# Optimization experiments

Measured on AMD Instinct MI355X. Metric: run time of the kernel, lower is better.

Reference implementation:

```python
import jax, jax.numpy as jnp
import numpy as np

SHRINK_THRES = 0.0025
EPS_SHRINK = 1e-12
EPS_NORM = 1e-12


def setup_inputs() -> dict:
    key = jax.random.key(0)
    k1, k2 = jax.random.split(key)
    B, C, H, W = 32, 256, 32, 32
    mem_dim, fea_dim = 2000, 256
    x = jax.random.normal(k1, (B, C, H, W), dtype=jnp.float32)
    stdv = 1.0 / np.sqrt(fea_dim)
    memMatrix = jax.random.uniform(k2, (mem_dim, fea_dim), dtype=jnp.float32,
                                   minval=-stdv, maxval=stdv)
    return {"x": x, "memMatrix": memMatrix}


def _hard_shrink_relu(a, lambd, eps=EPS_SHRINK):
    # relu(a - lambd) * a / (|a - lambd| + eps)
    return jax.nn.relu(a - lambd) * a / (jnp.abs(a - lambd) + eps)


def reference(x, memMatrix):
    B, C, H, W = x.shape
    mem_dim = memMatrix.shape[0]
    # [B,C,H,W] -> [B,H,W,C] -> [N,C]
    q = jnp.transpose(x, (0, 2, 3, 1)).reshape(-1, C)
    # attention addressing: [N, mem_dim]
    att = q @ memMatrix.T
    att = jax.nn.softmax(att, axis=1)
    # hard shrinkage + L1 renormalize
    att = _hard_shrink_relu(att, SHRINK_THRES)
    denom = jnp.maximum(jnp.sum(jnp.abs(att), axis=1, keepdims=True), EPS_NORM)
    att = att / denom
    # memory read: [N, C]
    out = att @ memMatrix
    # reshape back: y [B,C,H,W], att [B,mem_dim,H,W]
    y = jnp.transpose(out.reshape(B, H, W, C), (0, 3, 1, 2))
    att_map = jnp.transpose(att.reshape(B, H, W, mem_dim), (0, 3, 1, 2))
    return y, att_map
```

## Files before the change

kernel.cpp:

```cpp
#include <hip/hip_runtime.h>

#define B_   32
#define C_   256
#define HW_  1024
#define N_   32768
#define M_   2000
#define MP_  2048
#define K_   256

typedef __attribute__((ext_vector_type(8))) _Float16 f16x8;
typedef __attribute__((ext_vector_type(4))) float f32x4;

#define KCAP 32
#define AP   264

#define MFMA16(a, b, c) __builtin_amdgcn_mfma_f32_16x16x32_f16(a, b, c, 0, 0, 0)

__global__ void prep_memS_kernel(const float* __restrict__ mem,
                                 _Float16* __restrict__ mhs) {
  int m = blockIdx.x;
  int p = threadIdx.x;
  int c = ((p & 15) << 4) | (p >> 4);
  float v = (m < M_) ? mem[m * K_ + c] * 64.0f : 0.0f;
  _Float16 h = (_Float16)v;
  _Float16 l = (_Float16)(v - (float)h);
  int ks = p >> 5, kk = p & 31;
  int sh = (kk >> 3) ^ (m & 7);
  int sl = ((kk >> 3) + 4) ^ (m & 7);
  size_t base = ((size_t)ks * MP_ + m) * 64;
  mhs[base + sh * 8 + (kk & 7)] = h;
  mhs[base + sl * 8 + (kk & 7)] = l;
}

__global__ __launch_bounds__(512, 1) void fused_kernel(
    const float* __restrict__ x, const _Float16* __restrict__ mhs,
    const float* __restrict__ mem,
    float* __restrict__ y, float* __restrict__ att) {
  __shared__ _Float16 Bs[2][256 * 64];
  __shared__ _Float16 Ahs[32][AP];
  __shared__ _Float16 Als[32][AP];
  __shared__ float S_part[8][32];
  __shared__ float Sthr[32];
  __shared__ float inv_s[32];
  __shared__ unsigned int kcnt[32];
  __shared__ unsigned int km[32][KCAP];
  __shared__ float kp[32][KCAP];

  const int tid   = threadIdx.x;
  const int lane  = tid & 63;
  const int wave  = tid >> 6;
  const int row16 = lane & 15;
  const int quad  = lane >> 4;
  const int r7    = row16 & 7;
  const int n0  = blockIdx.x * 32;
  const int b   = n0 >> 10;
  const int hw0 = n0 & 1023;

  float (*xs)[33] = (float (*)[33])&Bs[0][0];

  {
    const int c = tid >> 1;
    const int h16 = (tid & 1) * 16;
    const float* src = x + ((size_t)b * C_ + c) * HW_ + hw0 + h16;
#pragma unroll
    for (int i = 0; i < 4; ++i)
      *(f32x4*)(&xs[c][h16 + i * 4]) = *(const f32x4*)(src + i * 4);
  }
  if (tid < 32) kcnt[tid] = 0;
  __syncthreads();

  {
    const int nl = tid >> 4;
    const int g  = tid & 15;
    f16x8 hi0, hi1, lo0, lo1;
#pragma unroll
    for (int u = 0; u < 8; ++u) {
      float v = xs[u * 16 + g][nl];
      _Float16 h = (_Float16)v;
      hi0[u] = h; lo0[u] = (_Float16)(v - (float)h);
    }
#pragma unroll
    for (int u = 0; u < 8; ++u) {
      float v = xs[(u + 8) * 16 + g][nl];
      _Float16 h = (_Float16)v;
      hi1[u] = h; lo1[u] = (_Float16)(v - (float)h);
    }
    *(f16x8*)(&Ahs[nl][g * 16])     = hi0;
    *(f16x8*)(&Ahs[nl][g * 16 + 8]) = hi1;
    *(f16x8*)(&Als[nl][g * 16])     = lo0;
    *(f16x8*)(&Als[nl][g * 16 + 8]) = lo1;
  }
  __syncthreads();

#define STAGE(bufidx, unit) do {                                              \
    const _Float16* gs_ = mhs + (size_t)(unit) * 16384;                       \
    _Float16* ld_ = &Bs[bufidx][0];                                           \
    _Pragma("unroll")                                                         \
    for (int i_ = 0; i_ < 4; ++i_) {                                          \
      __builtin_amdgcn_global_load_lds(                                       \
        (const __attribute__((address_space(1))) unsigned int*)(gs_ + (i_ * 512 + tid) * 8), \
        (__attribute__((address_space(3))) unsigned int*)(ld_ + (i_ * 512 + tid) * 8),       \
        16, 0, 0);                                                            \
    }                                                                         \
  } while (0)

  STAGE(0, 0);
  __syncthreads();

  f32x4 acc[8][2][2];
#pragma unroll
  for (int ch = 0; ch < 8; ++ch)
#pragma unroll
    for (int nf = 0; nf < 2; ++nf)
#pragma unroll
      for (int mf = 0; mf < 2; ++mf) acc[ch][nf][mf] = (f32x4){0.f, 0.f, 0.f, 0.f};

  const int mA = wave * 32;
  const int sH = (quad ^ r7) * 8;
  const int sL = ((4 | quad) ^ r7) * 8;

#pragma unroll 1
  for (int ks = 0; ks < 8; ++ks) {
    f16x8 ah[2], al[2];
#pragma unroll
    for (int nf = 0; nf < 2; ++nf) {
      ah[nf] = *(const f16x8*)(&Ahs[nf * 16 + row16][ks * 32 + quad * 8]);
      al[nf] = *(const f16x8*)(&Als[nf * 16 + row16][ks * 32 + quad * 8]);
    }
#pragma unroll
    for (int ch = 0; ch < 8; ++ch) {
      if (ch < 7) { STAGE((ch + 1) & 1, ks * 8 + ch + 1); }
      else if (ks < 7) { STAGE((ch + 1) & 1, ks * 8 + ch + 1); }
      const _Float16* bp0 = &Bs[ch & 1][(mA + row16) * 64];
      f16x8 bh0 = *(const f16x8*)(bp0 + sH);
      f16x8 bl0 = *(const f16x8*)(bp0 + sL);
      f16x8 bh1 = *(const f16x8*)(bp0 + 16 * 64 + sH);
      f16x8 bl1 = *(const f16x8*)(bp0 + 16 * 64 + sL);
      acc[ch][0][0] = MFMA16(ah[0], bh0, acc[ch][0][0]);
      acc[ch][1][0] = MFMA16(ah[1], bh0, acc[ch][1][0]);
      acc[ch][0][1] = MFMA16(ah[0], bh1, acc[ch][0][1]);
      acc[ch][1][1] = MFMA16(ah[1], bh1, acc[ch][1][1]);
      acc[ch][0][0] = MFMA16(al[0], bh0, acc[ch][0][0]);
      acc[ch][1][0] = MFMA16(al[1], bh0, acc[ch][1][0]);
      acc[ch][0][1] = MFMA16(al[0], bh1, acc[ch][0][1]);
      acc[ch][1][1] = MFMA16(al[1], bh1, acc[ch][1][1]);
      acc[ch][0][0] = MFMA16(ah[0], bl0, acc[ch][0][0]);
      acc[ch][1][0] = MFMA16(ah[1], bl0, acc[ch][1][0]);
      acc[ch][0][1] = MFMA16(ah[0], bl1, acc[ch][0][1]);
      acc[ch][1][1] = MFMA16(ah[1], bl1, acc[ch][1][1]);
      __syncthreads();
    }
  }

#pragma unroll
  for (int ch = 0; ch < 8; ++ch)
#pragma unroll
    for (int mf = 0; mf < 2; ++mf) {
      const bool valid = (ch * 256 + mA + mf * 16) < M_;
#pragma unroll
      for (int nf = 0; nf < 2; ++nf)
#pragma unroll
        for (int r = 0; r < 4; ++r)
          acc[ch][nf][mf][r] = valid ? __expf(acc[ch][nf][mf][r] * 0.015625f) : 0.f;
    }

  const int nlb = quad * 4;
#pragma unroll
  for (int nf = 0; nf < 2; ++nf)
#pragma unroll
    for (int r = 0; r < 4; ++r) {
      float s = 0.f;
#pragma unroll
      for (int ch = 0; ch < 8; ++ch)
        s += acc[ch][nf][0][r] + acc[ch][nf][1][r];
      s += __shfl_xor(s, 1, 16);
      s += __shfl_xor(s, 2, 16);
      s += __shfl_xor(s, 4, 16);
      s += __shfl_xor(s, 8, 16);
      if (row16 == 0) S_part[wave][nf * 16 + nlb + r] = s;
    }
  __syncthreads();
  if (tid < 32) {
    float s = 0.f;
#pragma unroll
    for (int w = 0; w < 8; ++w) s += S_part[w][tid];
    Sthr[tid] = 0.0025f * s;
  }
  __syncthreads();

#pragma unroll
  for (int nf = 0; nf < 2; ++nf)
#pragma unroll
    for (int r = 0; r < 4; ++r) {
      const int nl = nf * 16 + nlb + r;
      const float thr = Sthr[nl];
      float s2 = 0.f;
#pragma unroll
      for (int ch = 0; ch < 8; ++ch)
#pragma unroll
        for (int mf = 0; mf < 2; ++mf) {
          const float e = acc[ch][nf][mf][r];
          if (e > thr) {
            s2 += e;
            unsigned int pos = atomicAdd(&kcnt[nl], 1u);
            if (pos < (unsigned)KCAP) {
              km[nl][pos] = (unsigned)(ch * 256 + mA + mf * 16 + row16);
              kp[nl][pos] = e;
            }
          }
        }
      s2 += __shfl_xor(s2, 1, 16);
      s2 += __shfl_xor(s2, 2, 16);
      s2 += __shfl_xor(s2, 4, 16);
      s2 += __shfl_xor(s2, 8, 16);
      if (row16 == 0) S_part[wave][nl] = s2;
    }
  __syncthreads();
  if (tid < 32) {
    float s2 = 0.f;
#pragma unroll
    for (int w = 0; w < 8; ++w) s2 += S_part[w][tid];
    inv_s[tid] = (s2 > 0.f) ? 1.0f / s2 : 0.f;
  }
  __syncthreads();

  {
    f32x4 thr4[2], iv4[2];
#pragma unroll
    for (int nf = 0; nf < 2; ++nf)
#pragma unroll
      for (int r = 0; r < 4; ++r) {
        thr4[nf][r] = Sthr[nf * 16 + nlb + r];
        iv4[nf][r]  = inv_s[nf * 16 + nlb + r];
      }
    float* attb = att + (size_t)b * M_ * HW_ + hw0;
#pragma unroll
    for (int ch = 0; ch < 8; ++ch)
#pragma unroll
      for (int mf = 0; mf < 2; ++mf) {
        if (ch * 256 + mA + mf * 16 < M_) {
          const int m = ch * 256 + mA + mf * 16 + row16;
          float* ar = attb + (size_t)m * HW_ + nlb;
          f32x4 p0, p1;
#pragma unroll
          for (int r = 0; r < 4; ++r) {
            const float e0 = acc[ch][0][mf][r];
            const float e1 = acc[ch][1][mf][r];
            p0[r] = (e0 > thr4[0][r]) ? e0 * iv4[0][r] : 0.f;
            p1[r] = (e1 > thr4[1][r]) ? e1 * iv4[1][r] : 0.f;
          }
          *(f32x4*)(ar)      = p0;
          *(f32x4*)(ar + 16) = p1;
        }
      }
  }

  {
    const int hwL = tid & 31;
    const int cq  = tid >> 5;
    unsigned int kc = kcnt[hwL];
    if (kc > (unsigned)KCAP) kc = KCAP;
    const float iv = inv_s[hwL];
    float yv[16];
#pragma unroll
    for (int ci = 0; ci < 16; ++ci) yv[ci] = 0.f;
#pragma unroll 1
    for (unsigned int k = 0; k < kc; ++k) {
      const float p = kp[hwL][k];
      const float* mrow = mem + (size_t)km[hwL][k] * K_ + cq;
#pragma unroll
      for (int ci = 0; ci < 16; ++ci)
        yv[ci] += p * mrow[ci * 16];
    }
    float* yb = y + (size_t)b * C_ * HW_ + hw0 + hwL;
#pragma unroll
    for (int ci = 0; ci < 16; ++ci)
      yb[(size_t)(ci * 16 + cq) * HW_] = yv[ci] * iv;
  }
#undef STAGE
}

extern "C" void kernel_launch(void* const* d_in, const int* in_sizes, int n_in,
                              void* d_out, int out_size, void* d_ws, size_t ws_size,
                              hipStream_t stream) {
  const float* x   = (const float*)d_in[0];
  const float* mem = (const float*)d_in[1];
  float* y       = (float*)d_out;
  float* att_out = (float*)d_out + (size_t)B_ * C_ * HW_;

  _Float16* mhs = (_Float16*)d_ws;

  prep_memS_kernel<<<dim3(MP_), dim3(K_), 0, stream>>>(mem, mhs);
  fused_kernel<<<dim3(N_ / 32), dim3(512), 0, stream>>>(
      x, mhs, mem, y, att_out);
}
```

Measured before the change: 533.7 us.

## Halve B staging tiles and alias x/A buffers to raise occupancy

Shrinks the per-stage memory tile from 256 to 128 rows, so each wave computes one 16-row fragment per chunk over 16 chunks, and overlays the x transpose buffer with the hi/lo A buffers in a single shared region. Launch bounds move from 1 to 4 blocks per CU so several workgroups can hide the GEMM and the large att store latency. The first B stage is now issued before the x load to overlap it with the transpose. In exchange there are twice as many pipeline steps and barriers, and each B fragment is reused across fewer MFMAs.

New measurement: 671.7 us. 25.9% more time.

```diff
diff --git a/kernel.cpp b/kernel.cpp
--- a/kernel.cpp
+++ b/kernel.cpp
@@ -32,19 +32,22 @@
   mhs[base + sl * 8 + (kk & 7)] = l;
 }
 
-__global__ __launch_bounds__(512, 1) void fused_kernel(
+__global__ __launch_bounds__(512, 4) void fused_kernel(
     const float* __restrict__ x, const _Float16* __restrict__ mhs,
     const float* __restrict__ mem,
     float* __restrict__ y, float* __restrict__ att) {
-  __shared__ _Float16 Bs[2][256 * 64];
-  __shared__ _Float16 Ahs[32][AP];
-  __shared__ _Float16 Als[32][AP];
+  __shared__ _Float16 Bs[2][128 * 64];
+  __shared__ __align__(16) char axbuf[33792];
   __shared__ float S_part[8][32];
   __shared__ float Sthr[32];
   __shared__ float inv_s[32];
   __shared__ unsigned int kcnt[32];
   __shared__ unsigned int km[32][KCAP];
   __shared__ float kp[32][KCAP];
+
+  float    (*xs)[33]  = (float    (*)[33])axbuf;
+  _Float16 (*Ahs)[AP] = (_Float16 (*)[AP])axbuf;
+  _Float16 (*Als)[AP] = (_Float16 (*)[AP])(axbuf + 16896);
 
   const int tid   = threadIdx.x;
   const int lane  = tid & 63;
@@ -56,7 +59,20 @@
   const int b   = n0 >> 10;
   const int hw0 = n0 & 1023;
 
-  float (*xs)[33] = (float (*)[33])&Bs[0][0];
+#define STAGE(bufidx, unit) do {                                              \
+    const _Float16* gs_ = mhs + (size_t)(unit) * 8192;                        \
+    _Float16* ld_ = &Bs[bufidx][0];                                           \
+    __builtin_amdgcn_global_load_lds(                                         \
+      (const __attribute__((address_space(1))) unsigned int*)(gs_ + tid * 8), \
+      (__attribute__((address_space(3))) unsigned int*)(ld_ + tid * 8),       \
+      16, 0, 0);                                                              \
+    __builtin_amdgcn_global_load_lds(                                         \
+      (const __attribute__((address_space(1))) unsigned int*)(gs_ + (512 + tid) * 8), \
+      (__attribute__((address_space(3))) unsigned int*)(ld_ + (512 + tid) * 8),       \
+      16, 0, 0);                                                              \
+  } while (0)
+
+  STAGE(0, 0);
 
   {
     const int c = tid >> 1;
@@ -72,18 +88,20 @@
   {
     const int nl = tid >> 4;
     const int g  = tid & 15;
+    float v[16];
+#pragma unroll
+    for (int u = 0; u < 16; ++u) v[u] = xs[u * 16 + g][nl];
+    __syncthreads();
     f16x8 hi0, hi1, lo0, lo1;
 #pragma unroll
     for (int u = 0; u < 8; ++u) {
-      float v = xs[u * 16 + g][nl];
-      _Float16 h = (_Float16)v;
-      hi0[u] = h; lo0[u] = (_Float16)(v - (float)h);
+      _Float16 h = (_Float16)v[u];
+      hi0[u] = h; lo0[u] = (_Float16)(v[u] - (float)h);
     }
 #pragma unroll
     for (int u = 0; u < 8; ++u) {
-      float v = xs[(u + 8) * 16 + g][nl];
-      _Float16 h = (_Float16)v;
-      hi1[u] = h; lo1[u] = (_Float16)(v - (float)h);
+      _Float16 h = (_Float16)v[u + 8];
+      hi1[u] = h; lo1[u] = (_Float16)(v[u + 8] - (float)h);
     }
     *(f16x8*)(&Ahs[nl][g * 16])     = hi0;
     *(f16x8*)(&Ahs[nl][g * 16 + 8]) = hi1;
@@ -92,30 +110,13 @@
   }
   __syncthreads();
 
-#define STAGE(bufidx, unit) do {                                              \
-    const _Float16* gs_ = mhs + (size_t)(unit) * 16384;                       \
-    _Float16* ld_ = &Bs[bufidx][0];                                           \
-    _Pragma("unroll")                                                         \
-    for (int i_ = 0; i_ < 4; ++i_) {                                          \
-      __builtin_amdgcn_global_load_lds(                                       \
-        (const __attribute__((address_space(1))) unsigned int*)(gs_ + (i_ * 512 + tid) * 8), \
-        (__attribute__((address_space(3))) unsigned int*)(ld_ + (i_ * 512 + tid) * 8),       \
-        16, 0, 0);                                                            \
-    }                                                                         \
-  } while (0)
-
-  STAGE(0, 0);
-  __syncthreads();
-
-  f32x4 acc[8][2][2];
-#pragma unroll
-  for (int ch = 0; ch < 8; ++ch)
-#pragma unroll
-    for (int nf = 0; nf < 2; ++nf)
-#pragma unroll
-      for (int mf = 0; mf < 2; ++mf) acc[ch][nf][mf] = (f32x4){0.f, 0.f, 0.f, 0.f};
-
-  const int mA = wave * 32;
+  f32x4 acc[16][2];
+#pragma unroll
+  for (int ch = 0; ch < 16; ++ch)
+#pragma unroll
+    for (int nf = 0; nf < 2; ++nf) acc[ch][nf] = (f32x4){0.f, 0.f, 0.f, 0.f};
+
+  const int mA = wave * 16;
   const int sH = (quad ^ r7) * 8;
   const int sL = ((4 | quad) ^ r7) * 8;
 
@@ -128,41 +129,31 @@
       al[nf] = *(const f16x8*)(&Als[nf * 16 + row16][ks * 32 + quad * 8]);
     }
 #pragma unroll
-    for (int ch = 0; ch < 8; ++ch) {
-      if (ch < 7) { STAGE((ch + 1) & 1, ks * 8 + ch + 1); }
-      else if (ks < 7) { STAGE((ch + 1) & 1, ks * 8 + ch + 1); }
-      const _Float16* bp0 = &Bs[ch & 1][(mA + row16) * 64];
-      f16x8 bh0 = *(const f16x8*)(bp0 + sH);
-      f16x8 bl0 = *(const f16x8*)(bp0 + sL);
-      f16x8 bh1 = *(const f16x8*)(bp0 + 16 * 64 + sH);
-      f16x8 bl1 = *(const f16x8*)(bp0 + 16 * 64 + sL);
-      acc[ch][0][0] = MFMA16(ah[0], bh0, acc[ch][0][0]);
-      acc[ch][1][0] = MFMA16(ah[1], bh0, acc[ch][1][0]);
-      acc[ch][0][1] = MFMA16(ah[0], bh1, acc[ch][0][1]);
-      acc[ch][1][1] = MFMA16(ah[1], bh1, acc[ch][1][1]);
-      acc[ch][0][0] = MFMA16(al[0], bh0, acc[ch][0][0]);
-      acc[ch][1][0] = MFMA16(al[1], bh0, acc[ch][1][0]);
-      acc[ch][0][1] = MFMA16(al[0], bh1, acc[ch][0][1]);
-      acc[ch][1][1] = MFMA16(al[1], bh1, acc[ch][1][1]);
-      acc[ch][0][0] = MFMA16(ah[0], bl0, acc[ch][0][0]);
-      acc[ch][1][0] = MFMA16(ah[1], bl0, acc[ch][1][0]);
-      acc[ch][0][1] = MFMA16(ah[0], bl1, acc[ch][0][1]);
-      acc[ch][1][1] = MFMA16(ah[1], bl1, acc[ch][1][1]);
+    for (int ch = 0; ch < 16; ++ch) {
+      const int u = ks * 16 + ch;
+      if (u < 127) STAGE((u + 1) & 1, u + 1);
+      const _Float16* bp = &Bs[u & 1][(mA + row16) * 64];
+      f16x8 bh = *(const f16x8*)(bp + sH);
+      f16x8 bl = *(const f16x8*)(bp + sL);
+      acc[ch][0] = MFMA16(ah[0], bh, acc[ch][0]);
+      acc[ch][1] = MFMA16(ah[1], bh, acc[ch][1]);
+      acc[ch][0] = MFMA16(al[0], bh, acc[ch][0]);
+      acc[ch][1] = MFMA16(al[1], bh, acc[ch][1]);
+      acc[ch][0] = MFMA16(ah[0], bl, acc[ch][0]);
+      acc[ch][1] = MFMA16(ah[1], bl, acc[ch][1]);
       __syncthreads();
     }
   }
 
 #pragma unroll
-  for (int ch = 0; ch < 8; ++ch)
-#pragma unroll
-    for (int mf = 0; mf < 2; ++mf) {
-      const bool valid = (ch * 256 + mA + mf * 16) < M_;
-#pragma unroll
-      for (int nf = 0; nf < 2; ++nf)
-#pragma unroll
-        for (int r = 0; r < 4; ++r)
-          acc[ch][nf][mf][r] = valid ? __expf(acc[ch][nf][mf][r] * 0.015625f) : 0.f;
-    }
+  for (int ch = 0; ch < 16; ++ch) {
+    const bool valid = (ch * 128 + mA) < M_;
+#pragma unroll
+    for (int nf = 0; nf < 2; ++nf)
+#pragma unroll
+      for (int r = 0; r < 4; ++r)
+        acc[ch][nf][r] = valid ? __expf(acc[ch][nf][r] * 0.015625f) : 0.f;
+  }
 
   const int nlb = quad * 4;
 #pragma unroll
@@ -171,8 +162,7 @@
     for (int r = 0; r < 4; ++r) {
       float s = 0.f;
 #pragma unroll
-      for (int ch = 0; ch < 8; ++ch)
-        s += acc[ch][nf][0][r] + acc[ch][nf][1][r];
+      for (int ch = 0; ch < 16; ++ch) s += acc[ch][nf][r];
       s += __shfl_xor(s, 1, 16);
       s += __shfl_xor(s, 2, 16);
       s += __shfl_xor(s, 4, 16);
@@ -196,19 +186,17 @@
       const float thr = Sthr[nl];
       float s2 = 0.f;
 #pragma unroll
-      for (int ch = 0; ch < 8; ++ch)
-#pragma unroll
-        for (int mf = 0; mf < 2; ++mf) {
-          const float e = acc[ch][nf][mf][r];
-          if (e > thr) {
-            s2 += e;
-            unsigned int pos = atomicAdd(&kcnt[nl], 1u);
-            if (pos < (unsigned)KCAP) {
-              km[nl][pos] = (unsigned)(ch * 256 + mA + mf * 16 + row16);
-              kp[nl][pos] = e;
-            }
+      for (int ch = 0; ch < 16; ++ch) {
+        const float e = acc[ch][nf][r];
+        if (e > thr) {
+          s2 += e;
+          unsigned int pos = atomicAdd(&kcnt[nl], 1u);
+          if (pos < (unsigned)KCAP) {
+            km[nl][pos] = (unsigned)(ch * 128 + mA + row16);
+            kp[nl][pos] = e;
           }
         }
+      }
       s2 += __shfl_xor(s2, 1, 16);
       s2 += __shfl_xor(s2, 2, 16);
       s2 += __shfl_xor(s2, 4, 16);
@@ -235,24 +223,22 @@
       }
     float* attb = att + (size_t)b * M_ * HW_ + hw0;
 #pragma unroll
-    for (int ch = 0; ch < 8; ++ch)
-#pragma unroll
-      for (int mf = 0; mf < 2; ++mf) {
-        if (ch * 256 + mA + mf * 16 < M_) {
-          const int m = ch * 256 + mA + mf * 16 + row16;
-          float* ar = attb + (size_t)m * HW_ + nlb;
-          f32x4 p0, p1;
-#pragma unroll
-          for (int r = 0; r < 4; ++r) {
-            const float e0 = acc[ch][0][mf][r];
-            const float e1 = acc[ch][1][mf][r];
-            p0[r] = (e0 > thr4[0][r]) ? e0 * iv4[0][r] : 0.f;
-            p1[r] = (e1 > thr4[1][r]) ? e1 * iv4[1][r] : 0.f;
-          }
-          *(f32x4*)(ar)      = p0;
-          *(f32x4*)(ar + 16) = p1;
+    for (int ch = 0; ch < 16; ++ch) {
+      if (ch * 128 + mA < M_) {
+        const int m = ch * 128 + mA + row16;
+        float* ar = attb + (size_t)m * HW_ + nlb;
+        f32x4 p0, p1;
+#pragma unroll
+        for (int r = 0; r < 4; ++r) {
+          const float e0 = acc[ch][0][r];
+          const float e1 = acc[ch][1][r];
+          p0[r] = (e0 > thr4[0][r]) ? e0 * iv4[0][r] : 0.f;
+          p1[r] = (e1 > thr4[1][r]) ? e1 * iv4[1][r] : 0.f;
         }
+        *(f32x4*)(ar)      = p0;
+        *(f32x4*)(ar + 16) = p1;
       }
+    }
   }
 
   {
```
